# Kernel tuning notes

Measured on AMD Instinct MI355X. Metric: run time of the kernel, lower is better.

Reference implementation:

```python
import jax, jax.numpy as jnp
import numpy as np

MARGIN = 0.4
SCALE = 80.0
NEG_FILL = -1e30  # used instead of -inf for masked logsumexp (keeps grads NaN-free)

N, D, NUM_CLASSES = 8192, 128, 512


def setup_inputs() -> dict:
    key = jax.random.key(0)
    k1, k2 = jax.random.split(key)
    embeds = jax.random.normal(k1, (N, D), dtype=jnp.float32)
    labels = jax.random.randint(k2, (N,), 0, NUM_CLASSES, dtype=jnp.int64)
    return {"embeds": embeds, "labels": labels}


def _masked_lse(terms, mask):
    # stable logsumexp over axis=1 restricted to mask
    t = jnp.where(mask, terms, NEG_FILL)
    m = jnp.max(t, axis=1, keepdims=True)
    return jnp.squeeze(m, 1) + jnp.log(jnp.sum(jnp.exp(t - m), axis=1))


def reference(embeds, labels):
    # L2-normalize embeddings (F.normalize, p=2, dim=1, eps=1e-12)
    norm = jnp.maximum(jnp.linalg.norm(embeds, axis=1, keepdims=True), 1e-12)
    e = embeds / norm
    sim = e @ e.T  # [N, N]

    same = labels[:, None] == labels[None, :]
    eye = jnp.eye(labels.shape[0], dtype=bool)
    pos_mask = same & ~eye          # positives for each anchor (row)
    neg_mask = ~same                # negatives for each anchor

    # alphas are computed under no_grad in the original
    ap_alpha = jax.lax.stop_gradient(jax.nn.relu(1.0 + MARGIN - sim))
    an_alpha = jax.lax.stop_gradient(jax.nn.relu(sim + MARGIN))

    ap_term = -SCALE * ap_alpha * (sim - 1.0 + MARGIN)
    an_term = SCALE * an_alpha * (sim - MARGIN)

    np_cnt = jnp.sum(pos_mask, axis=1)  # positives per anchor
    nn_cnt = jnp.sum(neg_mask, axis=1)  # negatives per anchor
    valid = (np_cnt > 0) & (nn_cnt > 0)

    # All-triplets logsumexp factorizes: LSE over (p,n) pairs of ap_term[p]
    # equals LSE over p + log(num_neg); symmetric for an_term.
    lse_p = _masked_lse(ap_term, pos_mask)
    lse_n = _masked_lse(an_term, neg_mask)
    log_np = jnp.where(valid, jnp.log(np_cnt.astype(sim.dtype)), 0.0)
    log_nn = jnp.where(valid, jnp.log(nn_cnt.astype(sim.dtype)), 0.0)

    loss_i = jax.nn.softplus(lse_p + log_nn + lse_n + log_np)
    loss = jnp.sum(jnp.where(valid, loss_i, 0.0)) / jnp.maximum(
        jnp.sum(valid).astype(sim.dtype), 1.0)
    return loss
```

## Files before the change

kernel.cpp:

```cpp
#include <hip/hip_runtime.h>
#include <hip/hip_bf16.h>

#define NN_ 8192
#define DD_ 128
#define NSPLIT 16
#define JSPLIT (NN_ / NSPLIT)
#define MAINB 512
#define NCLS 512
#define CAP 48

typedef short bf16x8 __attribute__((ext_vector_type(8)));
typedef float f32x4 __attribute__((ext_vector_type(4)));
union U4 { uint4 u; bf16x8 h; };

#if __has_builtin(__builtin_amdgcn_exp2f)
#define EXP2(x) __builtin_amdgcn_exp2f(x)
#else
#define EXP2(x) __expf((x) * 0.69314718056f)
#endif

#define C1 115.415603f
#define LN2 0.69314718056f

__device__ __forceinline__ unsigned short f2bf(float f) {
    unsigned int u = __float_as_uint(f);
    unsigned int r = (u + 0x7FFFu + ((u >> 16) & 1u)) >> 16;
    return (unsigned short)r;
}


__global__ __launch_bounds__(256) void k_norm(const float* __restrict__ x,
                                              unsigned short* __restrict__ ebf,
                                              unsigned int* __restrict__ zinit) {
    int t = threadIdx.x;
    int r16 = t >> 4;
    int g = t & 15;
    int row = blockIdx.x * 16 + r16;
    const float4* xr = (const float4*)(x + (size_t)row * DD_);
    float4 v0 = xr[g * 2];
    float4 v1 = xr[g * 2 + 1];
    float ss = v0.x * v0.x + v0.y * v0.y + v0.z * v0.z + v0.w * v0.w +
               v1.x * v1.x + v1.y * v1.y + v1.z * v1.z + v1.w * v1.w;
#pragma unroll
    for (int m = 1; m < 16; m <<= 1) ss += __shfl_xor(ss, m);
    float inv = 1.0f / fmaxf(sqrtf(ss), 1e-12f);
    float vs[8] = {v0.x, v0.y, v0.z, v0.w, v1.x, v1.y, v1.z, v1.w};
    unsigned int p[4];
#pragma unroll
    for (int k = 0; k < 4; k++) {
        unsigned short lo = f2bf(vs[2 * k] * inv);
        unsigned short hi = f2bf(vs[2 * k + 1] * inv);
        p[k] = (unsigned int)lo | ((unsigned int)hi << 16);
    }
    uint4 out = {p[0], p[1], p[2], p[3]};
    ((uint4*)ebf)[blockIdx.x * 256 + g * 16 + r16] = out;
    if (blockIdx.x == 0 && t < 3) zinit[t] = 0u;
}

__device__ __forceinline__ void epi(const f32x4& acc, float* S, bool diag,
                                    int lcol, int quad) {
    if (diag) {
#pragma unroll
        for (int r = 0; r < 4; r++) {
            float s = acc[r];
            float e = EXP2(fmaf(s * C1, s, -C1));
            if (lcol == quad * 4 + r) e = 0.0f;
            S[r] += e;
        }
    } else {
#pragma unroll
        for (int r = 0; r < 4; r++) {
            float s = acc[r];
            float e = EXP2(fmaf(s * C1, s, -C1));
            S[r] += e;
        }
    }
}

__global__ __launch_bounds__(512, 4) void k_fused(const unsigned short* __restrict__ ebf,
                                                  const int* __restrict__ labels,
                                                  float* __restrict__ states,
                                                  float* __restrict__ posout) {
    __shared__ int lmem[CAP];
    __shared__ int lcnt;
    __shared__ float lvec[CAP * 128];
    __shared__ float pairT[CAP * CAP];
    __shared__ float pairE[CAP * CAP];

    const int tid = threadIdx.x;
    const int bid = blockIdx.x;

    if (bid < MAINB) {
        const int lane = tid & 63;
        const int wave = tid >> 6;
        const int quad = lane >> 4;
        const int lcol = lane & 15;
        const int jsplit = bid & 15;
        const int by = bid >> 4;
        const int rowbase = by * 256 + wave * 32;
        const int j0 = jsplit * JSPLIT;

        const uint4* fb = (const uint4*)ebf;

        U4 afr[2][4];
#pragma unroll
        for (int h = 0; h < 2; h++)
#pragma unroll
            for (int kc = 0; kc < 4; kc++)
                afr[h][kc].u = fb[((rowbase >> 4) + h) * 256 + kc * 64 + lane];

        float S_an[8] = {0.f, 0.f, 0.f, 0.f, 0.f, 0.f, 0.f, 0.f};

        U4 b0[4], b1[4];
#pragma unroll
        for (int kc = 0; kc < 4; kc++) b0[kc].u = fb[(j0 >> 4) * 256 + kc * 64 + lane];
#pragma unroll
        for (int kc = 0; kc < 4; kc++) b1[kc].u = fb[((j0 + 16) >> 4) * 256 + kc * 64 + lane];

        const int NIT = JSPLIT / 32;
        for (int it = 0; it < NIT; ++it) {
            const int jt = j0 + it * 32;
            const int jp = (it + 1 < NIT) ? jt + 32 : j0;

            {
                f32x4 a0 = {0.f, 0.f, 0.f, 0.f}, a1 = {0.f, 0.f, 0.f, 0.f};
#pragma unroll
                for (int kc = 0; kc < 4; kc++)
                    a0 = __builtin_amdgcn_mfma_f32_16x16x32_bf16(afr[0][kc].h, b0[kc].h, a0, 0, 0, 0);
#pragma unroll
                for (int kc = 0; kc < 4; kc++)
                    a1 = __builtin_amdgcn_mfma_f32_16x16x32_bf16(afr[1][kc].h, b0[kc].h, a1, 0, 0, 0);
                epi(a0, S_an + 0, jt == rowbase, lcol, quad);
                epi(a1, S_an + 4, jt == rowbase + 16, lcol, quad);
            }
#pragma unroll
            for (int kc = 0; kc < 4; kc++) b0[kc].u = fb[(jp >> 4) * 256 + kc * 64 + lane];

            {
                f32x4 a0 = {0.f, 0.f, 0.f, 0.f}, a1 = {0.f, 0.f, 0.f, 0.f};
#pragma unroll
                for (int kc = 0; kc < 4; kc++)
                    a0 = __builtin_amdgcn_mfma_f32_16x16x32_bf16(afr[0][kc].h, b1[kc].h, a0, 0, 0, 0);
#pragma unroll
                for (int kc = 0; kc < 4; kc++)
                    a1 = __builtin_amdgcn_mfma_f32_16x16x32_bf16(afr[1][kc].h, b1[kc].h, a1, 0, 0, 0);
                epi(a0, S_an + 0, jt + 16 == rowbase, lcol, quad);
                epi(a1, S_an + 4, jt + 16 == rowbase + 16, lcol, quad);
            }
#pragma unroll
            for (int kc = 0; kc < 4; kc++) b1[kc].u = fb[((jp + 16) >> 4) * 256 + kc * 64 + lane];
        }

#pragma unroll
        for (int hr = 0; hr < 8; hr++)
#pragma unroll
            for (int m = 1; m < 16; m <<= 1) S_an[hr] += __shfl_xor(S_an[hr], m);

        if (lcol == 0) {
#pragma unroll
            for (int h = 0; h < 2; h++)
#pragma unroll
                for (int r = 0; r < 4; r++) {
                    int i = rowbase + h * 16 + quad * 4 + r;
                    states[(size_t)i * NSPLIT + jsplit] = S_an[h * 4 + r];
                }
        }
    } else {
        const int c = bid - MAINB;
        if (tid == 0) lcnt = 0;
        __syncthreads();
        for (int idx = tid; idx < NN_; idx += 512) {
            if (labels[idx] == c) {
                int p = atomicAdd(&lcnt, 1);
                if (p < CAP) lmem[p] = idx;
            }
        }
        __syncthreads();
        int cnt = min(lcnt, CAP);

        for (int k = tid; k < cnt * 128; k += 512) {
            int m = k >> 7, d = k & 127;
            int row = lmem[m];
            int unit = (row >> 4) * 256 + (d >> 3) * 16 + (row & 15);
            unsigned short hv = ebf[unit * 8 + (d & 7)];
            lvec[k] = __uint_as_float(((unsigned int)hv) << 16);
        }
        __syncthreads();

        int npair = cnt * cnt;
        for (int p = tid; p < npair; p += 512) {
            int a2 = p / cnt, b2 = p - a2 * cnt;
            if (a2 == b2) {
                pairT[p] = -1e30f;
                pairE[p] = 0.0f;
            } else {
                float s = 0.0f;
#pragma unroll 8
                for (int d = 0; d < 128; d++) s = fmaf(lvec[a2 * 128 + d], lvec[b2 * 128 + d], s);
                pairE[p] = EXP2(fmaf(s * C1, s, -C1));
                float al = fmaxf(1.4f - s, 0.0f) * (-C1);
                pairT[p] = al * (s - 0.6f);
            }
        }
        __syncthreads();

        if (tid < cnt) {
            float mx = -1e30f;
            for (int b2 = 0; b2 < cnt; b2++) mx = fmaxf(mx, pairT[tid * cnt + b2]);
            float sp = 0.0f, ss = 0.0f;
            for (int b2 = 0; b2 < cnt; b2++) {
                sp += EXP2(pairT[tid * cnt + b2] - mx);
                ss += pairE[tid * cnt + b2];
            }
            float4 o = {mx, sp, ss, (float)cnt};
            ((float4*)posout)[lmem[tid]] = o;
        }
    }
}

__global__ __launch_bounds__(256) void k_fin(const float* __restrict__ states,
                                             const float* __restrict__ posout,
                                             float* __restrict__ accum,
                                             unsigned int* __restrict__ ticket,
                                             float* __restrict__ out) {
    int i = blockIdx.x * 256 + threadIdx.x;
    float4 po = ((const float4*)posout)[i];
    float S = 0.0f;
#pragma unroll
    for (int k = 0; k < NSPLIT; k++) S += states[(size_t)i * NSPLIT + k];
    S -= po.z;
    int cnt = (int)po.w;
    int np = cnt - 1, nn = NN_ - cnt;
    float loss = 0.0f, v = 0.0f;
    if (np > 0 && nn > 0 && po.y > 0.0f && S > 0.0f) {
        float lse_p = LN2 * po.x + __logf(po.y);
        float lse_n = 67.2f + __logf(S);
        float z = lse_p + lse_n + __logf((float)np) + __logf((float)nn);
        loss = fmaxf(z, 0.0f) + log1pf(__expf(-fabsf(z)));
        v = 1.0f;
    }
#pragma unroll
    for (int m = 1; m < 64; m <<= 1) {
        loss += __shfl_xor(loss, m);
        v += __shfl_xor(v, m);
    }
    if ((threadIdx.x & 63) == 0) {
        atomicAdd(&accum[0], loss);
        atomicAdd(&accum[1], v);
    }
    __syncthreads();
    if (threadIdx.x == 0) {
        __threadfence();
        unsigned int old = atomicAdd(ticket, 1u);
        if (old == gridDim.x - 1) {
            float L = atomicAdd(&accum[0], 0.0f);
            float V = atomicAdd(&accum[1], 0.0f);
            out[0] = L / fmaxf(V, 1.0f);
        }
    }
}

extern "C" void kernel_launch(void* const* d_in, const int* in_sizes, int n_in,
                              void* d_out, int out_size, void* d_ws, size_t ws_size,
                              hipStream_t stream) {
    const float* embeds = (const float*)d_in[0];
    const int* labels = (const int*)d_in[1];
    float* out = (float*)d_out;

    char* ws = (char*)d_ws;
    unsigned short* ebf = (unsigned short*)ws;
    float* states = (float*)(ws + 2097152);
    float* posout = (float*)(ws + 2097152 + 524288);
    float* accum = (float*)(ws + 2097152 + 524288 + 131072);
    unsigned int* ticket = (unsigned int*)(ws + 2097152 + 524288 + 131072 + 8);

    k_norm<<<NN_ / 16, 256, 0, stream>>>(embeds, ebf, (unsigned int*)accum);
    k_fused<<<MAINB + NCLS, 512, 0, stream>>>(ebf, labels, states, posout);
    k_fin<<<NN_ / 256, 256, 0, stream>>>(states, posout, accum, ticket, out);
}
```

Measured before the change: 103.8 us.

## Move per-class positive pass into norm kernel and split main GEMM wider

The per-class positive-pair computation moves out of the fused GEMM kernel and into the normalization kernel. It recomputes the normalized bf16-rounded vectors directly from the fp32 input, so the GEMM kernel no longer carries a long tail of heavyweight class blocks with large shared memory. The main kernel now runs only the negative-sum GEMM and doubles the column split to 32, giving 1024 blocks for better load balance. The cost is that the norm kernel does redundant normalization work and a larger states buffer must be written and then reduced in the final kernel.

After: 104.8 us. No clear change (+1.0%).

```diff
diff --git a/kernel.cpp b/kernel.cpp
--- a/kernel.cpp
+++ b/kernel.cpp
@@ -3,11 +3,12 @@
 
 #define NN_ 8192
 #define DD_ 128
-#define NSPLIT 16
+#define NSPLIT 32
 #define JSPLIT (NN_ / NSPLIT)
-#define MAINB 512
+#define NORMB 512
 #define NCLS 512
 #define CAP 48
+#define LVP 132
 
 typedef short bf16x8 __attribute__((ext_vector_type(8)));
 typedef float f32x4 __attribute__((ext_vector_type(4)));
@@ -29,192 +30,206 @@
 }
 
 
-__global__ __launch_bounds__(256) void k_norm(const float* __restrict__ x,
-                                              unsigned short* __restrict__ ebf,
-                                              unsigned int* __restrict__ zinit) {
-    int t = threadIdx.x;
-    int r16 = t >> 4;
-    int g = t & 15;
-    int row = blockIdx.x * 16 + r16;
-    const float4* xr = (const float4*)(x + (size_t)row * DD_);
-    float4 v0 = xr[g * 2];
-    float4 v1 = xr[g * 2 + 1];
-    float ss = v0.x * v0.x + v0.y * v0.y + v0.z * v0.z + v0.w * v0.w +
-               v1.x * v1.x + v1.y * v1.y + v1.z * v1.z + v1.w * v1.w;
-#pragma unroll
-    for (int m = 1; m < 16; m <<= 1) ss += __shfl_xor(ss, m);
-    float inv = 1.0f / fmaxf(sqrtf(ss), 1e-12f);
-    float vs[8] = {v0.x, v0.y, v0.z, v0.w, v1.x, v1.y, v1.z, v1.w};
-    unsigned int p[4];
-#pragma unroll
-    for (int k = 0; k < 4; k++) {
-        unsigned short lo = f2bf(vs[2 * k] * inv);
-        unsigned short hi = f2bf(vs[2 * k + 1] * inv);
-        p[k] = (unsigned int)lo | ((unsigned int)hi << 16);
-    }
-    uint4 out = {p[0], p[1], p[2], p[3]};
-    ((uint4*)ebf)[blockIdx.x * 256 + g * 16 + r16] = out;
-    if (blockIdx.x == 0 && t < 3) zinit[t] = 0u;
-}
-
-__device__ __forceinline__ void epi(const f32x4& acc, float* S, bool diag,
-                                    int lcol, int quad) {
-    if (diag) {
-#pragma unroll
-        for (int r = 0; r < 4; r++) {
-            float s = acc[r];
-            float e = EXP2(fmaf(s * C1, s, -C1));
-            if (lcol == quad * 4 + r) e = 0.0f;
-            S[r] += e;
-        }
-    } else {
-#pragma unroll
-        for (int r = 0; r < 4; r++) {
-            float s = acc[r];
-            float e = EXP2(fmaf(s * C1, s, -C1));
-            S[r] += e;
-        }
-    }
-}
-
-__global__ __launch_bounds__(512, 4) void k_fused(const unsigned short* __restrict__ ebf,
+__global__ __launch_bounds__(256) void k_norm_pos(const float* __restrict__ x,
                                                   const int* __restrict__ labels,
-                                                  float* __restrict__ states,
-                                                  float* __restrict__ posout) {
+                                                  unsigned short* __restrict__ ebf,
+                                                  float* __restrict__ posout,
+                                                  unsigned int* __restrict__ zinit) {
     __shared__ int lmem[CAP];
     __shared__ int lcnt;
-    __shared__ float lvec[CAP * 128];
-    __shared__ float pairT[CAP * CAP];
-    __shared__ float pairE[CAP * CAP];
-
-    const int tid = threadIdx.x;
+    __shared__ float lvec[CAP * LVP];
+    __shared__ float pairS[CAP * CAP];
+
+    const int t = threadIdx.x;
     const int bid = blockIdx.x;
 
-    if (bid < MAINB) {
-        const int lane = tid & 63;
-        const int wave = tid >> 6;
-        const int quad = lane >> 4;
-        const int lcol = lane & 15;
-        const int jsplit = bid & 15;
-        const int by = bid >> 4;
-        const int rowbase = by * 256 + wave * 32;
-        const int j0 = jsplit * JSPLIT;
-
-        const uint4* fb = (const uint4*)ebf;
-
-        U4 afr[2][4];
+    if (bid < NORMB) {
+        int r16 = t >> 4;
+        int g = t & 15;
+        int row = bid * 16 + r16;
+        const float4* xr = (const float4*)(x + (size_t)row * DD_);
+        float4 v0 = xr[g * 2];
+        float4 v1 = xr[g * 2 + 1];
+        float ss = v0.x * v0.x + v0.y * v0.y + v0.z * v0.z + v0.w * v0.w +
+                   v1.x * v1.x + v1.y * v1.y + v1.z * v1.z + v1.w * v1.w;
+#pragma unroll
+        for (int m = 1; m < 16; m <<= 1) ss += __shfl_xor(ss, m);
+        float inv = 1.0f / fmaxf(sqrtf(ss), 1e-12f);
+        float vs[8] = {v0.x, v0.y, v0.z, v0.w, v1.x, v1.y, v1.z, v1.w};
+        unsigned int p[4];
+#pragma unroll
+        for (int k = 0; k < 4; k++) {
+            unsigned short lo = f2bf(vs[2 * k] * inv);
+            unsigned short hi = f2bf(vs[2 * k + 1] * inv);
+            p[k] = (unsigned int)lo | ((unsigned int)hi << 16);
+        }
+        uint4 out = {p[0], p[1], p[2], p[3]};
+        ((uint4*)ebf)[bid * 256 + g * 16 + r16] = out;
+        if (bid == 0 && t < 3) zinit[t] = 0u;
+        return;
+    }
+
+    const int c = bid - NORMB;
+    if (t == 0) lcnt = 0;
+    __syncthreads();
+    for (int idx = t; idx < NN_; idx += 256) {
+        if (labels[idx] == c) {
+            int p = atomicAdd(&lcnt, 1);
+            if (p < CAP) lmem[p] = idx;
+        }
+    }
+    __syncthreads();
+    int cnt = min(lcnt, CAP);
+
+    for (int base = 0; base < cnt; base += 16) {
+        int lr = base + (t >> 4);
+        int g = t & 15;
+        bool valid = lr < cnt;
+        int row = lmem[valid ? lr : 0];
+        const float4* xr = (const float4*)(x + (size_t)row * DD_);
+        float4 v0 = xr[g * 2];
+        float4 v1 = xr[g * 2 + 1];
+        float ss = v0.x * v0.x + v0.y * v0.y + v0.z * v0.z + v0.w * v0.w +
+                   v1.x * v1.x + v1.y * v1.y + v1.z * v1.z + v1.w * v1.w;
+#pragma unroll
+        for (int m = 1; m < 16; m <<= 1) ss += __shfl_xor(ss, m);
+        float inv = 1.0f / fmaxf(sqrtf(ss), 1e-12f);
+        if (valid) {
+            float vs[8] = {v0.x, v0.y, v0.z, v0.w, v1.x, v1.y, v1.z, v1.w};
+#pragma unroll
+            for (int k = 0; k < 8; k++) {
+                unsigned short h = f2bf(vs[k] * inv);
+                lvec[lr * LVP + g * 8 + k] = __uint_as_float(((unsigned int)h) << 16);
+            }
+        }
+    }
+    __syncthreads();
+
+    int npair = cnt * cnt;
+    for (int p = t; p < npair; p += 256) {
+        int a2 = p / cnt, b2 = p - a2 * cnt;
+        float s = 0.0f;
+#pragma unroll 16
+        for (int d = 0; d < 128; d++)
+            s = fmaf(lvec[a2 * LVP + d], lvec[b2 * LVP + d], s);
+        pairS[p] = s;
+    }
+    __syncthreads();
+
+    if (t < cnt) {
+        float mx = -1e30f;
+        for (int b2 = 0; b2 < cnt; b2++) {
+            if (b2 == t) continue;
+            float s = pairS[t * cnt + b2];
+            float al = fmaxf(1.4f - s, 0.0f) * (-C1);
+            mx = fmaxf(mx, al * (s - 0.6f));
+        }
+        float sp = 0.0f, ssum = 0.0f;
+        for (int b2 = 0; b2 < cnt; b2++) {
+            if (b2 == t) continue;
+            float s = pairS[t * cnt + b2];
+            float al = fmaxf(1.4f - s, 0.0f) * (-C1);
+            sp += EXP2(al * (s - 0.6f) - mx);
+            ssum += EXP2(fmaf(s * C1, s, -C1));
+        }
+        float4 o = {mx, sp, ssum, (float)cnt};
+        ((float4*)posout)[lmem[t]] = o;
+    }
+}
+
+__global__ __launch_bounds__(512, 4) void k_main(const unsigned short* __restrict__ ebf,
+                                                 float* __restrict__ states) {
+    const int lane = threadIdx.x & 63;
+    const int wave = threadIdx.x >> 6;
+    const int quad = lane >> 4;
+    const int lcol = lane & 15;
+    const int jsplit = blockIdx.x & 31;
+    const int by = blockIdx.x >> 5;
+    const int rowbase = by * 256 + wave * 32;
+    const int j0 = jsplit * JSPLIT;
+
+    const uint4* fb = (const uint4*)ebf;
+
+    U4 afr[2][4];
+#pragma unroll
+    for (int h = 0; h < 2; h++)
+#pragma unroll
+        for (int kc = 0; kc < 4; kc++)
+            afr[h][kc].u = fb[((rowbase >> 4) + h) * 256 + kc * 64 + lane];
+
+    float S_an[8] = {0.f, 0.f, 0.f, 0.f, 0.f, 0.f, 0.f, 0.f};
+
+    U4 b0[4], b1[4];
+#pragma unroll
+    for (int kc = 0; kc < 4; kc++) b0[kc].u = fb[(j0 >> 4) * 256 + kc * 64 + lane];
+#pragma unroll
+    for (int kc = 0; kc < 4; kc++) b1[kc].u = fb[((j0 + 16) >> 4) * 256 + kc * 64 + lane];
+
+    const int NIT = JSPLIT / 32;
+    for (int it = 0; it < NIT; ++it) {
+        const int jt = j0 + it * 32;
+        const int jp = (it + 1 < NIT) ? jt + 32 : j0;
+
+        {
+            f32x4 a0 = {0.f, 0.f, 0.f, 0.f}, a1 = {0.f, 0.f, 0.f, 0.f};
+#pragma unroll
+            for (int kc = 0; kc < 4; kc++)
+                a0 = __builtin_amdgcn_mfma_f32_16x16x32_bf16(afr[0][kc].h, b0[kc].h, a0, 0, 0, 0);
+#pragma unroll
+            for (int kc = 0; kc < 4; kc++)
+                a1 = __builtin_amdgcn_mfma_f32_16x16x32_bf16(afr[1][kc].h, b0[kc].h, a1, 0, 0, 0);
+            bool d0 = (jt == rowbase), d1 = (jt == rowbase + 16);
+#pragma unroll
+            for (int r = 0; r < 4; r++) {
+                float s0 = a0[r], s1 = a1[r];
+                float e0 = EXP2(fmaf(s0 * C1, s0, -C1));
+                float e1 = EXP2(fmaf(s1 * C1, s1, -C1));
+                if (d0 && lcol == quad * 4 + r) e0 = 0.0f;
+                if (d1 && lcol == quad * 4 + r) e1 = 0.0f;
+                S_an[r] += e0;
+                S_an[4 + r] += e1;
+            }
+        }
+#pragma unroll
+        for (int kc = 0; kc < 4; kc++) b0[kc].u = fb[(jp >> 4) * 256 + kc * 64 + lane];
+
+        {
+            f32x4 a0 = {0.f, 0.f, 0.f, 0.f}, a1 = {0.f, 0.f, 0.f, 0.f};
+#pragma unroll
+            for (int kc = 0; kc < 4; kc++)
+                a0 = __builtin_amdgcn_mfma_f32_16x16x32_bf16(afr[0][kc].h, b1[kc].h, a0, 0, 0, 0);
+#pragma unroll
+            for (int kc = 0; kc < 4; kc++)
+                a1 = __builtin_amdgcn_mfma_f32_16x16x32_bf16(afr[1][kc].h, b1[kc].h, a1, 0, 0, 0);
+            bool d0 = (jt + 16 == rowbase), d1 = (jt + 16 == rowbase + 16);
+#pragma unroll
+            for (int r = 0; r < 4; r++) {
+                float s0 = a0[r], s1 = a1[r];
+                float e0 = EXP2(fmaf(s0 * C1, s0, -C1));
+                float e1 = EXP2(fmaf(s1 * C1, s1, -C1));
+                if (d0 && lcol == quad * 4 + r) e0 = 0.0f;
+                if (d1 && lcol == quad * 4 + r) e1 = 0.0f;
+                S_an[r] += e0;
+                S_an[4 + r] += e1;
+            }
+        }
+#pragma unroll
+        for (int kc = 0; kc < 4; kc++) b1[kc].u = fb[((jp + 16) >> 4) * 256 + kc * 64 + lane];
+    }
+
+#pragma unroll
+    for (int hr = 0; hr < 8; hr++)
+#pragma unroll
+        for (int m = 1; m < 16; m <<= 1) S_an[hr] += __shfl_xor(S_an[hr], m);
+
+    if (lcol == 0) {
 #pragma unroll
         for (int h = 0; h < 2; h++)
 #pragma unroll
-            for (int kc = 0; kc < 4; kc++)
-                afr[h][kc].u = fb[((rowbase >> 4) + h) * 256 + kc * 64 + lane];
-
-        float S_an[8] = {0.f, 0.f, 0.f, 0.f, 0.f, 0.f, 0.f, 0.f};
-
-        U4 b0[4], b1[4];
-#pragma unroll
-        for (int kc = 0; kc < 4; kc++) b0[kc].u = fb[(j0 >> 4) * 256 + kc * 64 + lane];
-#pragma unroll
-        for (int kc = 0; kc < 4; kc++) b1[kc].u = fb[((j0 + 16) >> 4) * 256 + kc * 64 + lane];
-
-        const int NIT = JSPLIT / 32;
-        for (int it = 0; it < NIT; ++it) {
-            const int jt = j0 + it * 32;
-            const int jp = (it + 1 < NIT) ? jt + 32 : j0;
-
-            {
-                f32x4 a0 = {0.f, 0.f, 0.f, 0.f}, a1 = {0.f, 0.f, 0.f, 0.f};
-#pragma unroll
-                for (int kc = 0; kc < 4; kc++)
-                    a0 = __builtin_amdgcn_mfma_f32_16x16x32_bf16(afr[0][kc].h, b0[kc].h, a0, 0, 0, 0);
-#pragma unroll
-                for (int kc = 0; kc < 4; kc++)
-                    a1 = __builtin_amdgcn_mfma_f32_16x16x32_bf16(afr[1][kc].h, b0[kc].h, a1, 0, 0, 0);
-                epi(a0, S_an + 0, jt == rowbase, lcol, quad);
-                epi(a1, S_an + 4, jt == rowbase + 16, lcol, quad);
-            }
-#pragma unroll
-            for (int kc = 0; kc < 4; kc++) b0[kc].u = fb[(jp >> 4) * 256 + kc * 64 + lane];
-
-            {
-                f32x4 a0 = {0.f, 0.f, 0.f, 0.f}, a1 = {0.f, 0.f, 0.f, 0.f};
-#pragma unroll
-                for (int kc = 0; kc < 4; kc++)
-                    a0 = __builtin_amdgcn_mfma_f32_16x16x32_bf16(afr[0][kc].h, b1[kc].h, a0, 0, 0, 0);
-#pragma unroll
-                for (int kc = 0; kc < 4; kc++)
-                    a1 = __builtin_amdgcn_mfma_f32_16x16x32_bf16(afr[1][kc].h, b1[kc].h, a1, 0, 0, 0);
-                epi(a0, S_an + 0, jt + 16 == rowbase, lcol, quad);
-                epi(a1, S_an + 4, jt + 16 == rowbase + 16, lcol, quad);
-            }
-#pragma unroll
-            for (int kc = 0; kc < 4; kc++) b1[kc].u = fb[((jp + 16) >> 4) * 256 + kc * 64 + lane];
-        }
-
-#pragma unroll
-        for (int hr = 0; hr < 8; hr++)
-#pragma unroll
-            for (int m = 1; m < 16; m <<= 1) S_an[hr] += __shfl_xor(S_an[hr], m);
-
-        if (lcol == 0) {
-#pragma unroll
-            for (int h = 0; h < 2; h++)
-#pragma unroll
-                for (int r = 0; r < 4; r++) {
-                    int i = rowbase + h * 16 + quad * 4 + r;
-                    states[(size_t)i * NSPLIT + jsplit] = S_an[h * 4 + r];
-                }
-        }
-    } else {
-        const int c = bid - MAINB;
-        if (tid == 0) lcnt = 0;
-        __syncthreads();
-        for (int idx = tid; idx < NN_; idx += 512) {
-            if (labels[idx] == c) {
-                int p = atomicAdd(&lcnt, 1);
-                if (p < CAP) lmem[p] = idx;
-            }
-        }
-        __syncthreads();
-        int cnt = min(lcnt, CAP);
-
-        for (int k = tid; k < cnt * 128; k += 512) {
-            int m = k >> 7, d = k & 127;
-            int row = lmem[m];
-            int unit = (row >> 4) * 256 + (d >> 3) * 16 + (row & 15);
-            unsigned short hv = ebf[unit * 8 + (d & 7)];
-            lvec[k] = __uint_as_float(((unsigned int)hv) << 16);
-        }
-        __syncthreads();
-
-        int npair = cnt * cnt;
-        for (int p = tid; p < npair; p += 512) {
-            int a2 = p / cnt, b2 = p - a2 * cnt;
-            if (a2 == b2) {
-                pairT[p] = -1e30f;
-                pairE[p] = 0.0f;
-            } else {
-                float s = 0.0f;
-#pragma unroll 8
-                for (int d = 0; d < 128; d++) s = fmaf(lvec[a2 * 128 + d], lvec[b2 * 128 + d], s);
-                pairE[p] = EXP2(fmaf(s * C1, s, -C1));
-                float al = fmaxf(1.4f - s, 0.0f) * (-C1);
-                pairT[p] = al * (s - 0.6f);
-            }
-        }
-        __syncthreads();
-
-        if (tid < cnt) {
-            float mx = -1e30f;
-            for (int b2 = 0; b2 < cnt; b2++) mx = fmaxf(mx, pairT[tid * cnt + b2]);
-            float sp = 0.0f, ss = 0.0f;
-            for (int b2 = 0; b2 < cnt; b2++) {
-                sp += EXP2(pairT[tid * cnt + b2] - mx);
-                ss += pairE[tid * cnt + b2];
-            }
-            float4 o = {mx, sp, ss, (float)cnt};
-            ((float4*)posout)[lmem[tid]] = o;
-        }
+            for (int r = 0; r < 4; r++) {
+                int i = rowbase + h * 16 + quad * 4 + r;
+                states[(size_t)i * NSPLIT + jsplit] = S_an[h * 4 + r];
+            }
     }
 }
 
@@ -270,11 +285,12 @@
     char* ws = (char*)d_ws;
     unsigned short* ebf = (unsigned short*)ws;
     float* states = (float*)(ws + 2097152);
-    float* posout = (float*)(ws + 2097152 + 524288);
-    float* accum = (float*)(ws + 2097152 + 524288 + 131072);
-    unsigned int* ticket = (unsigned int*)(ws + 2097152 + 524288 + 131072 + 8);
-
-    k_norm<<<NN_ / 16, 256, 0, stream>>>(embeds, ebf, (unsigned int*)accum);
-    k_fused<<<MAINB + NCLS, 512, 0, stream>>>(ebf, labels, states, posout);
+    float* posout = (float*)(ws + 2097152 + 1048576);
+    float* accum = (float*)(ws + 2097152 + 1048576 + 131072);
+    unsigned int* ticket = (unsigned int*)(ws + 2097152 + 1048576 + 131072 + 8);
+
+    k_norm_pos<<<NORMB + NCLS, 256, 0, stream>>>(embeds, labels, ebf, posout,
+                                                 (unsigned int*)accum);
+    k_main<<<NN_ / 256 * NSPLIT, 512, 0, stream>>>(ebf, states);
     k_fin<<<NN_ / 256, 256, 0, stream>>>(states, posout, accum, ticket, out);
 }
```
